# Performance work log

Measured on AMD Instinct MI355X. Metric: run time of the kernel, lower is better.

## Reference

```python
import jax, jax.numpy as jnp
import numpy as np

NUM_QUBITS = 12
NUM_LAYERS = 2
STATE_DIM = 2 ** NUM_QUBITS
BATCH = 4096
TWO_PI = 2 * 3.1416  # matches the original initializer constant


def _u3(theta, phi, lam):
    """Single-qubit U3 gate, 2x2 complex64 (matches TF layer exactly)."""
    c = jnp.cos(theta / 2)
    s = jnp.sin(theta / 2)
    z = jnp.zeros_like(phi)
    e_phi = jnp.exp(jax.lax.complex(z, phi))
    e_lam = jnp.exp(jax.lax.complex(z, lam))
    e_pl = jnp.exp(jax.lax.complex(z, phi + lam))
    cc = jax.lax.complex(c, jnp.zeros_like(c))
    sc = jax.lax.complex(s, jnp.zeros_like(s))
    row1 = jnp.stack([cc, -e_lam * sc])
    row2 = jnp.stack([e_phi * sc, e_pl * cc])
    return jnp.stack([row1, row2])  # [2, 2] complex64


def _full_gate(theta_vec, phi_vec, lam_vec):
    """Kronecker product of per-qubit gates -> [2^n, 2^n] complex64."""
    full = _u3(theta_vec[0], phi_vec[0], lam_vec[0])
    for q in range(1, theta_vec.shape[0]):
        full = jnp.kron(full, _u3(theta_vec[q], phi_vec[q], lam_vec[q]))
    return full


def setup_inputs() -> dict:
    key = jax.random.key(0)
    k1, k2, k3, k4 = jax.random.split(key, 4)
    inputs = jax.random.normal(k1, (BATCH, STATE_DIM), dtype=jnp.float32)
    thetas = jax.random.uniform(k2, (NUM_LAYERS, NUM_QUBITS), minval=0.0, maxval=TWO_PI, dtype=jnp.float32)
    phis = jax.random.uniform(k3, (NUM_LAYERS, NUM_QUBITS), minval=0.0, maxval=TWO_PI, dtype=jnp.float32)
    lams = jax.random.uniform(k4, (NUM_LAYERS, NUM_QUBITS), minval=0.0, maxval=TWO_PI, dtype=jnp.float32)
    return {"inputs": inputs, "thetas": thetas, "phis": phis, "lams": lams}


def reference(inputs, thetas, phis, lams):
    # normalize real inputs as complex state, per-sample L2 norm
    state = jax.lax.complex(inputs, jnp.zeros_like(inputs))  # [B, D] complex64
    norm = jnp.linalg.norm(state, axis=1, keepdims=True)      # real, [B, 1]
    state = state / norm
    for l in range(thetas.shape[0]):
        U = _full_gate(thetas[l], phis[l], lams[l])  # [D, D]
        # matvec(U, x) per sample == state @ U^T, batched GEMM replaces tf.map_fn
        state = state @ U.T
    return jnp.real(state * jnp.conj(state))  # probabilities, [B, D] float32
```

## Files before the change

kernel.cpp:

```cpp
#include <hip/hip_runtime.h>

#define NQ   12
#define DIM  4096
#define NL   2
#define BATCH 4096

typedef float v2f __attribute__((ext_vector_type(2)));


struct PGate { v2f a00, b00, a01, b01, a10, b10, a11, b11; };

__global__ void build_gates(const float* __restrict__ th,
                            const float* __restrict__ ph,
                            const float* __restrict__ lm,
                            float* __restrict__ gates) {
    int q = threadIdx.x;
    if (q >= NQ) return;
    float g00r = 1.f, g00i = 0.f, g01r = 0.f, g01i = 0.f;
    float g10r = 0.f, g10i = 0.f, g11r = 1.f, g11i = 0.f;
    #pragma unroll
    for (int l = 0; l < NL; ++l) {
        float th2 = 0.5f * th[l * NQ + q];
        float p   = ph[l * NQ + q];
        float la  = lm[l * NQ + q];
        float s, c, sl, cl, sp, cp, spl, cpl;
        __sincosf(th2, &s, &c);
        __sincosf(la, &sl, &cl);
        __sincosf(p, &sp, &cp);
        __sincosf(p + la, &spl, &cpl);
        float u00r = c,        u00i = 0.f;
        float u01r = -cl * s,  u01i = -sl * s;
        float u10r = cp * s,   u10i = sp * s;
        float u11r = cpl * c,  u11i = spl * c;
        float n00r = u00r*g00r - u00i*g00i + u01r*g10r - u01i*g10i;
        float n00i = u00r*g00i + u00i*g00r + u01r*g10i + u01i*g10r;
        float n01r = u00r*g01r - u00i*g01i + u01r*g11r - u01i*g11i;
        float n01i = u00r*g01i + u00i*g01r + u01r*g11i + u01i*g11r;
        float n10r = u10r*g00r - u10i*g00i + u11r*g10r - u11i*g10i;
        float n10i = u10r*g00i + u10i*g00r + u11r*g10i + u11i*g10r;
        float n11r = u10r*g01r - u10i*g01i + u11r*g11r - u11i*g11i;
        float n11i = u10r*g01i + u10i*g01r + u11r*g11i + u11i*g11r;
        g00r = n00r; g00i = n00i; g01r = n01r; g01i = n01i;
        g10r = n10r; g10i = n10i; g11r = n11r; g11i = n11i;
    }
    int k = (NQ - 1) - q;
    float* o = gates + k * 16;
    o[0]  = g00r;  o[1]  = g00i;  o[2]  = -g00i; o[3]  = g00r;
    o[4]  = g01r;  o[5]  = g01i;  o[6]  = -g01i; o[7]  = g01r;
    o[8]  = g10r;  o[9]  = g10i;  o[10] = -g10i; o[11] = g10r;
    o[12] = g11r;  o[13] = g11i;  o[14] = -g11i; o[15] = g11r;
}

__device__ __forceinline__ v2f blo(v2f x) { return __builtin_shufflevector(x, x, 0, 0); }
__device__ __forceinline__ v2f bhi(v2f x) { return __builtin_shufflevector(x, x, 1, 1); }

__device__ __forceinline__ void papply(v2f v[16], int r0, int r1, const PGate& g) {
    v2f x0 = v[r0], x1 = v[r1];
    v2f x0r = blo(x0), x0i = bhi(x0), x1r = blo(x1), x1i = bhi(x1);
    v[r0] = g.a00 * x0r + g.b00 * x0i + g.a01 * x1r + g.b01 * x1i;
    v[r1] = g.a10 * x0r + g.b10 * x0i + g.a11 * x1r + g.b11 * x1i;
}

__device__ __forceinline__ void papply_rbit(v2f v[16], int rb, const PGate& g) {
    const int m = 1 << rb;
    #pragma unroll
    for (int h = 0; h < 8; ++h) {
        int low = h & (m - 1);
        int r   = ((h & ~(m - 1)) << 1) | low;
        papply(v, r, r | m, g);
    }
}

__device__ __forceinline__ int lds_off(int idx) { return idx + (idx >> 4); }

__device__ __forceinline__ int map1(int r, int t) {
    return ((r >> 2) << 10) | (t << 2) | (r & 3);
}
__device__ __forceinline__ int map2(int r, int t) {
    return (t & 3) | ((r & 3) << 2) | (((r >> 2) & 3) << 4)
         | (((t >> 2) & 3) << 6) | (((t >> 6) & 3) << 8) | (((t >> 4) & 3) << 10);
}
__device__ __forceinline__ int map3(int r, int t) {
    return (t & 63) | (r << 6) | ((t >> 6) << 10);
}

__global__ __launch_bounds__(256, 4)
void qc_sim(const float* __restrict__ in,
            const PGate* __restrict__ gp,
            float* __restrict__ out) {
    __shared__ v2f   st[DIM + DIM / 16];
    __shared__ float red[4];

    const int t    = threadIdx.x;
    const int lane = t & 63;
    const int b    = blockIdx.x;

    const float4* __restrict__ x4 =
        reinterpret_cast<const float4*>(in + (size_t)b * DIM);
    float4 lA[4];
    #pragma unroll
    for (int j = 0; j < 4; ++j) lA[j] = x4[j * 256 + t];

    float ss = 0.f;
    #pragma unroll
    for (int j = 0; j < 4; ++j)
        ss += lA[j].x*lA[j].x + lA[j].y*lA[j].y + lA[j].z*lA[j].z + lA[j].w*lA[j].w;
    #pragma unroll
    for (int off = 32; off > 0; off >>= 1)
        ss += __shfl_down(ss, off, 64);
    if (lane == 0) red[t >> 6] = ss;

    v2f v[16];

    {
        PGate g0 = gp[0];
        #pragma unroll
        for (int j = 0; j < 4; ++j) {
            v2f x0, x1;
            x0 = (v2f){ lA[j].x, lA[j].x }; x1 = (v2f){ lA[j].y, lA[j].y };
            v[4*j]   = g0.a00 * x0 + g0.a01 * x1;  v[4*j+1] = g0.a10 * x0 + g0.a11 * x1;
            x0 = (v2f){ lA[j].z, lA[j].z }; x1 = (v2f){ lA[j].w, lA[j].w };
            v[4*j+2] = g0.a00 * x0 + g0.a01 * x1;  v[4*j+3] = g0.a10 * x0 + g0.a11 * x1;
        }
        { PGate g = gp[1];  papply_rbit(v, 1, g); }
        { PGate g = gp[10]; papply_rbit(v, 2, g); }
        { PGate g = gp[11]; papply_rbit(v, 3, g); }
    }

    #pragma unroll
    for (int r = 0; r < 16; ++r) st[lds_off(map1(r, t))] = v[r];
    #pragma unroll
    for (int r = 0; r < 16; ++r) v[r] = st[lds_off(map2(r, t))];

    { PGate g = gp[2]; papply_rbit(v, 0, g); }
    { PGate g = gp[3]; papply_rbit(v, 1, g); }
    { PGate g = gp[4]; papply_rbit(v, 2, g); }
    { PGate g = gp[5]; papply_rbit(v, 3, g); }

    #pragma unroll
    for (int r = 0; r < 16; ++r) st[lds_off(map2(r, t))] = v[r];
    __syncthreads();
    #pragma unroll
    for (int r = 0; r < 16; ++r) v[r] = st[lds_off(map3(r, t))];

    { PGate g = gp[6]; papply_rbit(v, 0, g); }
    { PGate g = gp[7]; papply_rbit(v, 1, g); }
    { PGate g = gp[8]; papply_rbit(v, 2, g); }
    { PGate g = gp[9]; papply_rbit(v, 3, g); }

    float inv = 1.0f / (red[0] + red[1] + red[2] + red[3]);
    float* __restrict__ o = out + (size_t)b * DIM;
    #pragma unroll
    for (int r = 0; r < 16; ++r) {
        v2f p2 = v[r] * v[r];
        o[map3(r, t)] = (p2.x + p2.y) * inv;
    }
}

extern "C" void kernel_launch(void* const* d_in, const int* in_sizes, int n_in,
                              void* d_out, int out_size, void* d_ws, size_t ws_size,
                              hipStream_t stream) {
    (void)in_sizes; (void)n_in; (void)out_size; (void)ws_size;
    const float* inputs = (const float*)d_in[0];
    const float* thetas = (const float*)d_in[1];
    const float* phis   = (const float*)d_in[2];
    const float* lams   = (const float*)d_in[3];
    float* gates = (float*)d_ws;
    float* out   = (float*)d_out;

    hipLaunchKernelGGL(build_gates, dim3(1), dim3(64), 0, stream,
                       thetas, phis, lams, gates);
    hipLaunchKernelGGL(qc_sim, dim3(BATCH), dim3(256), 0, stream,
                       inputs, (const PGate*)gates, out);
}
```

Baseline: 129.3 us.

## Store LDS exchange state as half2 and raise occupancy target

The shared-memory transpose buffer now holds the complex amplitudes as packed fp16 pairs instead of float2, halving LDS footprint and traffic. Launch bounds go from 4 to 8 blocks per CU to use the freed LDS, and the index maps are precomputed per thread with a new padding scheme. Gate-building sincos switches to precise versions. Rounding the intermediate state to half precision adds error to the output probabilities and may exceed tolerance. It also pressures registers harder under the higher occupancy bound.

```diff
diff --git a/kernel.cpp b/kernel.cpp
--- a/kernel.cpp
+++ b/kernel.cpp
@@ -1,4 +1,5 @@
 #include <hip/hip_runtime.h>
+#include <hip/hip_fp16.h>
 
 #define NQ   12
 #define DIM  4096
@@ -24,10 +25,10 @@
         float p   = ph[l * NQ + q];
         float la  = lm[l * NQ + q];
         float s, c, sl, cl, sp, cp, spl, cpl;
-        __sincosf(th2, &s, &c);
-        __sincosf(la, &sl, &cl);
-        __sincosf(p, &sp, &cp);
-        __sincosf(p + la, &spl, &cpl);
+        sincosf(th2, &s, &c);
+        sincosf(la, &sl, &cl);
+        sincosf(p, &sp, &cp);
+        sincosf(p + la, &spl, &cpl);
         float u00r = c,        u00i = 0.f;
         float u01r = -cl * s,  u01i = -sl * s;
         float u10r = cp * s,   u10i = sp * s;
@@ -71,24 +72,20 @@
     }
 }
 
-__device__ __forceinline__ int lds_off(int idx) { return idx + (idx >> 4); }
-
-__device__ __forceinline__ int map1(int r, int t) {
-    return ((r >> 2) << 10) | (t << 2) | (r & 3);
+__device__ __forceinline__ __half2 pack2(v2f x) {
+    return __floats2half2_rn(x.x, x.y);
 }
-__device__ __forceinline__ int map2(int r, int t) {
-    return (t & 3) | ((r & 3) << 2) | (((r >> 2) & 3) << 4)
-         | (((t >> 2) & 3) << 6) | (((t >> 6) & 3) << 8) | (((t >> 4) & 3) << 10);
-}
-__device__ __forceinline__ int map3(int r, int t) {
-    return (t & 63) | (r << 6) | ((t >> 6) << 10);
+__device__ __forceinline__ v2f unpack2(__half2 h) {
+    return (v2f){ __low2float(h), __high2float(h) };
 }
 
-__global__ __launch_bounds__(256, 4)
+#define LDS_N 4384
+
+__global__ __launch_bounds__(256, 8)
 void qc_sim(const float* __restrict__ in,
             const PGate* __restrict__ gp,
             float* __restrict__ out) {
-    __shared__ v2f   st[DIM + DIM / 16];
+    __shared__ __half2 st[LDS_N];
     __shared__ float red[4];
 
     const int t    = threadIdx.x;
@@ -127,10 +124,23 @@
         { PGate g = gp[11]; papply_rbit(v, 3, g); }
     }
 
+    const int A1 = (t << 2) + (t >> 2);
+    const int b2 = (t & 3) | (((t >> 2) & 3) << 6)
+                 | (((t >> 6) & 3) << 8) | (((t >> 4) & 3) << 10);
+    const int A2 = b2 + (b2 >> 4) + 9 * ((t >> 4) & 3);
+    const int b3 = (t & 63) | ((t >> 6) << 10);
+    const int A3 = b3 + (b3 >> 4) + 9 * (t >> 6);
+
     #pragma unroll
-    for (int r = 0; r < 16; ++r) st[lds_off(map1(r, t))] = v[r];
+    for (int r = 0; r < 16; ++r) {
+        const int K1 = ((r >> 2) << 10) + ((r >> 2) << 6) + 9 * (r >> 2) + (r & 3);
+        st[A1 + K1] = pack2(v[r]);
+    }
     #pragma unroll
-    for (int r = 0; r < 16; ++r) v[r] = st[lds_off(map2(r, t))];
+    for (int r = 0; r < 16; ++r) {
+        const int K2 = ((r & 3) << 2) + ((r >> 2) << 4) + (r >> 2);
+        v[r] = unpack2(st[A2 + K2]);
+    }
 
     { PGate g = gp[2]; papply_rbit(v, 0, g); }
     { PGate g = gp[3]; papply_rbit(v, 1, g); }
@@ -138,10 +148,13 @@
     { PGate g = gp[5]; papply_rbit(v, 3, g); }
 
     #pragma unroll
-    for (int r = 0; r < 16; ++r) st[lds_off(map2(r, t))] = v[r];
+    for (int r = 0; r < 16; ++r) {
+        const int K2 = ((r & 3) << 2) + ((r >> 2) << 4) + (r >> 2);
+        st[A2 + K2] = pack2(v[r]);
+    }
     __syncthreads();
     #pragma unroll
-    for (int r = 0; r < 16; ++r) v[r] = st[lds_off(map3(r, t))];
+    for (int r = 0; r < 16; ++r) v[r] = unpack2(st[A3 + 68 * r]);
 
     { PGate g = gp[6]; papply_rbit(v, 0, g); }
     { PGate g = gp[7]; papply_rbit(v, 1, g); }
@@ -153,7 +166,7 @@
     #pragma unroll
     for (int r = 0; r < 16; ++r) {
         v2f p2 = v[r] * v[r];
-        o[map3(r, t)] = (p2.x + p2.y) * inv;
+        o[b3 + (r << 6)] = (p2.x + p2.y) * inv;
     }
 }
 
```

Result: slower. 134.2 us (+3.8%).
